# Optimization experiments

Hardware: AMD Instinct MI355X
Metric: run time of the kernel (lower is better)

The kernel has to match this reference:

```python
import jax, jax.numpy as jnp
import numpy as np

H = 128          # hidden_channels
K = 3            # TAGConv hops
NV, NS = 100000, 50000
EVV, ESS, EH, EIN = 1_000_000, 500_000, 500_000, 300_000


def setup_inputs() -> dict:
    key = jax.random.key(0)
    ks = iter(jax.random.split(key, 40))
    def rn(shape, s=0.05):
        return jax.random.normal(next(ks), shape, jnp.float32) * s
    def ri(shape, hi):
        return jax.random.randint(next(ks), shape, 0, hi, jnp.int32)
    return {
        "game_x": rn((NV, 5), 1.0),
        "state_x": rn((NS, 6), 1.0),
        "edge_index_v_v": ri((2, EVV), NV),
        "edge_type_v_v": ri((EVV,), 4),  # unused in forward (interface fidelity)
        "edge_index_history_v_s": jnp.stack([ri((EH,), NV), ri((EH,), NS)]),
        "edge_attr_history_v_s": rn((EH, 1), 1.0),
        "edge_index_in_v_s": jnp.stack([ri((EIN,), NV), ri((EIN,), NS)]),
        "edge_index_s_s": ri((2, ESS), NS),
        # TAGConv weights: (K+1) hop linears, shared bias
        "tag1_W": rn((K + 1, 5, H)), "tag1_b": rn((H,)),
        "tag2_W": rn((K + 1, 6, H)), "tag2_b": rn((H,)),
        # 7 SAGEConv layers stacked: gv[1:3]=0,1; sv[1:3]=2,3; in1=4; sv2=5,6
        "sage_Wl": rn((7, H, H)), "sage_bl": rn((7, H)), "sage_Wr": rn((7, H, H)),
        # GATConv (1 head, edge_dim=1)
        "gat_Wsrc": rn((H, H)), "gat_Wdst": rn((H, H)), "gat_We": rn((1, H)),
        "gat_asrc": rn((H,)), "gat_adst": rn((H,)), "gat_ae": rn((H,)), "gat_b": rn((H,)),
        # final MLP: single Linear(H, 1)
        "mlp_W": rn((H, 1)), "mlp_b": rn((1,)),
    }


def _seg_sum(x, idx, n):
    return jax.ops.segment_sum(x, idx, num_segments=n)


def tag_conv(x, edge_index, n, W, b):
    """TAGConv: out = sum_k lin_k(A_norm^k x) + b, gcn_norm w/o self loops."""
    src, dst = edge_index[0], edge_index[1]
    deg = _seg_sum(jnp.ones(src.shape, x.dtype), dst, n)
    dinv = jnp.where(deg > 0, jax.lax.rsqrt(jnp.maximum(deg, 1.0)), 0.0)
    norm = dinv[src] * dinv[dst]                      # [E]
    out = x @ W[0]
    h = x
    for k in range(1, W.shape[0]):
        h = _seg_sum(h[src] * norm[:, None], dst, n)  # one hop of normalized A
        out = out + h @ W[k]
    return out + b


def sage_conv(x_src, x_dst, edge_index, n_dst, Wl, bl, Wr):
    """SAGEConv(mean): lin_l(mean_j x_src[j]) + lin_r(x_dst)."""
    src, dst = edge_index[0], edge_index[1]
    s = _seg_sum(x_src[src], dst, n_dst)
    cnt = _seg_sum(jnp.ones(src.shape, x_src.dtype), dst, n_dst)
    mean = s / jnp.maximum(cnt, 1.0)[:, None]
    return mean @ Wl + bl + x_dst @ Wr


def gat_conv(x_src, x_dst, edge_index, edge_attr, n_dst,
             Wsrc, Wdst, We, asrc, adst, ae, b):
    """Bipartite GATConv, 1 head, edge features, no self loops."""
    src, dst = edge_index[0], edge_index[1]
    hs = x_src @ Wsrc                                  # [NV, H]
    hd = x_dst @ Wdst                                  # [NS, H]
    a = (hs @ asrc)[src] + (hd @ adst)[dst] + (edge_attr @ We) @ ae  # [E]
    a = jax.nn.leaky_relu(a, 0.2)
    m = jax.ops.segment_max(a, dst, num_segments=n_dst)
    e = jnp.exp(a - m[dst])                            # segment softmax
    denom = _seg_sum(e, dst, n_dst)
    alpha = e / jnp.maximum(denom, 1e-16)[dst]
    out = _seg_sum(alpha[:, None] * hs[src], dst, n_dst)
    return out + b


def reference(game_x, state_x, edge_index_v_v, edge_type_v_v,
              edge_index_history_v_s, edge_attr_history_v_s,
              edge_index_in_v_s, edge_index_s_s,
              tag1_W, tag1_b, tag2_W, tag2_b,
              sage_Wl, sage_bl, sage_Wr,
              gat_Wsrc, gat_Wdst, gat_We, gat_asrc, gat_adst, gat_ae, gat_b,
              mlp_W, mlp_b):
    relu = jax.nn.relu
    nv, ns = game_x.shape[0], state_x.shape[0]
    # game-vertex tower
    gx = relu(tag_conv(game_x, edge_index_v_v, nv, tag1_W, tag1_b))
    for i in range(2):
        gx = relu(sage_conv(gx, gx, edge_index_v_v, nv, sage_Wl[i], sage_bl[i], sage_Wr[i]))
    # state-vertex tower
    sx = relu(tag_conv(state_x, edge_index_s_s, ns, tag2_W, tag2_b))
    for i in range(2, 4):
        sx = relu(sage_conv(sx, sx, edge_index_s_s, ns, sage_Wl[i], sage_bl[i], sage_Wr[i]))
    # bipartite attention game -> state
    hist = relu(gat_conv(gx, sx, edge_index_history_v_s, edge_attr_history_v_s, ns,
                         gat_Wsrc, gat_Wdst, gat_We, gat_asrc, gat_adst, gat_ae, gat_b))
    in_x = relu(sage_conv(gx, hist, edge_index_in_v_s, ns, sage_Wl[4], sage_bl[4], sage_Wr[4]))
    # second state tower
    sx = in_x
    for i in range(5, 7):
        sx = relu(sage_conv(sx, sx, edge_index_s_s, ns, sage_Wl[i], sage_bl[i], sage_Wr[i]))
    return sx @ mlp_W + mlp_b                          # [NS, 1]
```

## Files before the change

### kernel.cpp

```cpp
#include <hip/hip_runtime.h>

#define H 128
typedef unsigned short u16;
typedef __attribute__((ext_vector_type(8))) short bf16x8;
typedef __attribute__((ext_vector_type(4))) float f32x4;


static inline int gridFor(long long work, int block, int cap = 8192){
  long long g = (work + block - 1) / block;
  if (g > cap) g = cap;
  if (g < 1) g = 1;
  return (int)g;
}

__device__ __forceinline__ float waveReduceSum(float v){
  #pragma unroll
  for(int off = 32; off > 0; off >>= 1) v += __shfl_down(v, off);
  return v;
}

__device__ __forceinline__ float bflo(unsigned v){ return __uint_as_float(v << 16); }
__device__ __forceinline__ float bfhi(unsigned v){ return __uint_as_float(v & 0xffff0000u); }
__device__ __forceinline__ u16 f2bf(float f){
  unsigned u = __float_as_uint(f);
  return (u16)((u + 0x7fffu + ((u >> 16) & 1u)) >> 16);
}
__device__ __forceinline__ unsigned pack2(float lo, float hi){
  return (unsigned)f2bf(lo) | ((unsigned)f2bf(hi) << 16);
}

#define BSHIFT 9
#define CH 2048

template<bool HAS_ATTR>
__global__ __launch_bounds__(256) void part_kernel(
    const int* __restrict__ src, const int* __restrict__ dst,
    const float* __restrict__ attr, int* __restrict__ bcur,
    int2* __restrict__ bpairs, float* __restrict__ battr, int E, int cap){
  __shared__ int hist[256];
  __shared__ int hscan[256];
  __shared__ int hbase[256];
  __shared__ int hcur[256];
  __shared__ int2 buf[CH];
  __shared__ float abuf[HAS_ATTR ? CH : 1];

  const int t = threadIdx.x;
  const int e0 = blockIdx.x * CH;
  const int cnt = min(CH, E - e0);

  hist[t] = 0; hcur[t] = 0;
  __syncthreads();

  #pragma unroll
  for(int j = 0; j < 8; j++){
    int i = e0 + j*256 + t;
    if(i - e0 < cnt) atomicAdd(&hist[dst[i] >> BSHIFT], 1);
  }
  __syncthreads();

  {
    int v = hist[t];
    int lane = t & 63, wid = t >> 6;
    int incl = v;
    #pragma unroll
    for(int off = 1; off < 64; off <<= 1){
      int u = __shfl_up(incl, off);
      if(lane >= off) incl += u;
    }
    __shared__ int ws4[4];
    if(lane == 63) ws4[wid] = incl;
    __syncthreads();
    int wofs = 0;
    for(int wj = 0; wj < wid; wj++) wofs += ws4[wj];
    hscan[t] = wofs + incl - v;
    hbase[t] = (v > 0) ? atomicAdd(&bcur[t], v) : 0;
  }
  __syncthreads();

  #pragma unroll
  for(int j = 0; j < 8; j++){
    int i = e0 + j*256 + t;
    if(i - e0 < cnt){
      int d = dst[i], s = src[i];
      int b = d >> BSHIFT;
      int lp = atomicAdd(&hcur[b], 1);
      int slot = hscan[b] + lp;
      buf[slot] = make_int2(d, s);
      if(HAS_ATTR) abuf[slot] = attr[i];
    }
  }
  __syncthreads();

  for(int u = t; u < cnt; u += 256){
    int2 pr = buf[u];
    int b = pr.x >> BSHIFT;
    int g = b * cap + hbase[b] + (u - hscan[b]);
    bpairs[g] = pr;
    if(HAS_ATTR) battr[g] = abuf[u];
  }
}

__global__ void bucket_scan(const int* __restrict__ bcur, int* __restrict__ bbase,
                            int* __restrict__ rp0, int* __restrict__ rp1,
                            int* __restrict__ rp2, int* __restrict__ rp3,
                            int n0, int n1, int n2, int n3){
  int g = blockIdx.x;
  int n = (g == 0) ? n0 : (g == 1) ? n1 : (g == 2) ? n2 : n3;
  int* rowp = (g == 0) ? rp0 : (g == 1) ? rp1 : (g == 2) ? rp2 : rp3;
  int NB = (n + 511) >> BSHIFT;
  int t = threadIdx.x;
  int v = (t < NB) ? bcur[g*256 + t] : 0;
  int lane = t & 63, wid = t >> 6;
  int incl = v;
  #pragma unroll
  for(int off = 1; off < 64; off <<= 1){
    int u = __shfl_up(incl, off);
    if(lane >= off) incl += u;
  }
  __shared__ int ws4[4];
  if(lane == 63) ws4[wid] = incl;
  __syncthreads();
  int wofs = 0;
  for(int wj = 0; wj < wid; wj++) wofs += ws4[wj];
  bbase[g*256 + t] = wofs + incl - v;
  if(t == 0) rowp[n] = ws4[0] + ws4[1] + ws4[2] + ws4[3];
}

template<bool HAS_ATTR, bool DINV>
__global__ __launch_bounds__(256) void build_kernel(
    const int2* __restrict__ bpairs, const float* __restrict__ battr,
    const int* __restrict__ bcur, const int* __restrict__ bbase,
    int* __restrict__ rowp, int* __restrict__ col, float* __restrict__ attrp,
    float* __restrict__ dinv, int cap, int n){
  __shared__ int hist[512];
  __shared__ int hcur[512];
  __shared__ int ws4[4];

  const int b = blockIdx.x;
  const int t = threadIdx.x;
  const int d0 = b << BSHIFT;
  const int dn = min(512, n - d0);
  const int cnt = bcur[b];
  const int base = bbase[b];
  const int2* ep = bpairs + (size_t)b * cap;

  hist[t] = 0; hist[t + 256] = 0;
  __syncthreads();
  for(int u = t; u < cnt; u += 256) atomicAdd(&hist[ep[u].x - d0], 1);
  __syncthreads();

  int a0 = hist[2*t], a1 = hist[2*t + 1];
  int s = a0 + a1;
  int lane = t & 63, wid = t >> 6;
  int incl = s;
  #pragma unroll
  for(int off = 1; off < 64; off <<= 1){
    int u = __shfl_up(incl, off);
    if(lane >= off) incl += u;
  }
  if(lane == 63) ws4[wid] = incl;
  __syncthreads();
  int wofs = 0;
  for(int wj = 0; wj < wid; wj++) wofs += ws4[wj];
  int excl = wofs + incl - s;
  __syncthreads();
  hcur[2*t] = excl; hcur[2*t + 1] = excl + a0;
  if(2*t < dn){
    rowp[d0 + 2*t] = base + excl;
    if(DINV) dinv[d0 + 2*t] = a0 > 0 ? rsqrtf((float)a0) : 0.f;
  }
  if(2*t + 1 < dn){
    rowp[d0 + 2*t + 1] = base + excl + a0;
    if(DINV) dinv[d0 + 2*t + 1] = a1 > 0 ? rsqrtf((float)a1) : 0.f;
  }
  __syncthreads();

  for(int u = t; u < cnt; u += 256){
    int2 pr = ep[u];
    int pos = base + atomicAdd(&hcur[pr.x - d0], 1);
    col[pos] = pr.y;
    if(HAS_ATTR) attrp[pos] = battr[(size_t)b * cap + u];
  }
}


__global__ void cvt_weights(const float* __restrict__ Wl, const float* __restrict__ Wr,
                            const float* __restrict__ Wsrc, u16* __restrict__ Wb){
  const int total = 15 * H * H;
  for(int t = blockIdx.x*blockDim.x + threadIdx.x; t < total; t += gridDim.x*blockDim.x){
    int mat = t >> 14, idx = t & 16383;
    int k = idx >> 7, colj = idx & 127;
    const float* srcp = (mat < 7) ? (Wl + ((size_t)mat << 14))
                       : (mat < 14) ? (Wr + ((size_t)(mat - 7) << 14))
                       : Wsrc;
    Wb[((size_t)mat << 14) + (size_t)colj*H + k] = f2bf(srcp[idx]);
  }
}

__global__ void mat_vec_row(const float* __restrict__ W, const float* __restrict__ a,
                            float* __restrict__ outv){
  int k = threadIdx.x;
  if(k < H){
    float s = 0.f;
    for(int j = 0; j < H; j++) s += W[(size_t)k*H + j] * a[j];
    outv[k] = s;
  }
}

__global__ void dot128(const float* __restrict__ a, const float* __restrict__ b,
                       float* __restrict__ o){
  int l = threadIdx.x;
  float acc = a[l]*b[l] + a[l+64]*b[l+64];
  acc = waveReduceSum(acc);
  if(l == 0) o[0] = acc;
}


template<int C>
__global__ void csr_tag_hop(const int* __restrict__ rowp, const int* __restrict__ col,
                            const float* __restrict__ dinv,
                            const float* __restrict__ hin, int sin,
                            float* __restrict__ hout, int sout, int N){
  for(int i = blockIdx.x*blockDim.x + threadIdx.x; i < N; i += gridDim.x*blockDim.x){
    int b = rowp[i], e = rowp[i+1];
    float dd = dinv[i];
    float acc0[C], acc1[C];
    #pragma unroll
    for(int k = 0; k < C; k++){ acc0[k] = 0.f; acc1[k] = 0.f; }
    int p = b;
    for(; p + 2 <= e; p += 2){
      int s0 = col[p], s1 = col[p+1];
      float n0 = dinv[s0] * dd, n1 = dinv[s1] * dd;
      #pragma unroll
      for(int k = 0; k < C; k++){
        acc0[k] += hin[(size_t)s0*sin + k] * n0;
        acc1[k] += hin[(size_t)s1*sin + k] * n1;
      }
    }
    if(p < e){
      int s0 = col[p];
      float n0 = dinv[s0] * dd;
      #pragma unroll
      for(int k = 0; k < C; k++) acc0[k] += hin[(size_t)s0*sin + k] * n0;
    }
    #pragma unroll
    for(int k = 0; k < C; k++) hout[(size_t)i*sout + k] = acc0[k] + acc1[k];
  }
}

template<int C>
__global__ __launch_bounds__(256) void tag_fuse(
    const float* __restrict__ x, const float* __restrict__ hcat,
    const float* __restrict__ W, const float* __restrict__ bias,
    u16* __restrict__ out, int N){
  __shared__ float Ws[4*C*H];
  for(int u = threadIdx.x; u < 4*C*H; u += 256) Ws[u] = W[u];
  __syncthreads();
  const long long total = (long long)N * H;
  for(long long t = (long long)blockIdx.x*blockDim.x + threadIdx.x; t < total;
      t += (long long)gridDim.x*blockDim.x){
    int i = (int)(t >> 7), j = (int)(t & 127);
    const float* xr = x + (size_t)i*C;
    const float* hr = hcat + (size_t)i*3*C;
    float acc = bias[j];
    #pragma unroll
    for(int k = 0; k < C; k++) acc += xr[k] * Ws[k*H + j];
    #pragma unroll
    for(int k = 0; k < 3*C; k++) acc += hr[k] * Ws[(C + k)*H + j];
    out[t] = f2bf(fmaxf(acc, 0.f));
  }
}


__global__ void csr_gather(const int* __restrict__ rowp, const int* __restrict__ col,
                           const u16* __restrict__ x, u16* __restrict__ agg, int N){
  int lane = threadIdx.x & 63;
  int w = (blockIdx.x*blockDim.x + threadIdx.x) >> 6;
  int nw = (gridDim.x*blockDim.x) >> 6;
  for(int i = w; i < N; i += nw){
    int b = rowp[i], e = rowp[i+1];
    float xs[8], ys[8];
    #pragma unroll
    for(int j = 0; j < 8; j++){ xs[j] = 0.f; ys[j] = 0.f; }
    int p = b;
    for(; p + 8 <= e; p += 8){
      unsigned v[8];
      #pragma unroll
      for(int j = 0; j < 8; j++)
        v[j] = *(const unsigned*)&x[(size_t)col[p + j]*H + lane*2];
      #pragma unroll
      for(int j = 0; j < 8; j++){ xs[j] += bflo(v[j]); ys[j] += bfhi(v[j]); }
    }
    for(; p < e; p++){
      unsigned v = *(const unsigned*)&x[(size_t)col[p]*H + lane*2];
      xs[0] += bflo(v); ys[0] += bfhi(v);
    }
    float sx = (xs[0]+xs[1])+(xs[2]+xs[3])+((xs[4]+xs[5])+(xs[6]+xs[7]));
    float sy = (ys[0]+ys[1])+(ys[2]+ys[3])+((ys[4]+ys[5])+(ys[6]+ys[7]));
    float inv = 1.f / fmaxf((float)(e - b), 1.f);
    *(unsigned*)&agg[(size_t)i*H + lane*2] = pack2(sx*inv, sy*inv);
  }
}


template<bool HAS_AGG, bool RELU, bool BIAS>
__global__ __launch_bounds__(256) void combine_mfma(
    const u16* __restrict__ x, const u16* __restrict__ agg,
    const u16* __restrict__ WbR, const u16* __restrict__ WbL,
    const float* __restrict__ bl, u16* __restrict__ out, int N){
  __shared__ u16 Ws[(HAS_AGG ? 2 : 1) * H * H];

  #pragma unroll
  for(int m = 0; m < (HAS_AGG ? 2 : 1); m++){
    const u16* Wp = m ? WbL : WbR;
    char* dst = (char*)(Ws + m * H * H);
    for(int u = threadIdx.x; u < H * H / 8; u += 256){
      bf16x8 v = *(const bf16x8*)&Wp[u * 8];
      int c  = u >> 4;
      int kb = (u & 15) * 16;
      *(bf16x8*)(dst + c * 256 + (kb ^ ((c & 7) << 4))) = v;
    }
  }
  __syncthreads();

  const int lane = threadIdx.x & 63;
  const int wib  = threadIdx.x >> 6;
  const int m0   = (blockIdx.x * 4 + wib) * 32;
  if(m0 >= N) return;
  const int r16 = lane & 15;
  const int kg  = (lane >> 4) * 8;

  f32x4 acc[2][8];
  #pragma unroll
  for(int rt = 0; rt < 2; rt++)
    #pragma unroll
    for(int t = 0; t < 8; t++) acc[rt][t] = (f32x4){0.f, 0.f, 0.f, 0.f};

  #pragma unroll
  for(int phase = 0; phase < (HAS_AGG ? 2 : 1); phase++){
    const u16* Ap = phase ? agg : x;
    const char* Wbase = (const char*)(Ws + phase * H * H);
    #pragma unroll
    for(int k0 = 0; k0 < H; k0 += 32){
      bf16x8 af[2];
      #pragma unroll
      for(int rt = 0; rt < 2; rt++){
        int row = m0 + rt * 16 + r16;
        if(row < N) af[rt] = *(const bf16x8*)&Ap[(size_t)row * H + k0 + kg];
        else        af[rt] = (bf16x8){0,0,0,0,0,0,0,0};
      }
      #pragma unroll
      for(int t = 0; t < 8; t++){
        int c = t * 16 + r16;
        int kb = (k0 + kg) * 2;
        bf16x8 bf = *(const bf16x8*)(Wbase + c * 256 + (kb ^ ((c & 7) << 4)));
        acc[0][t] = __builtin_amdgcn_mfma_f32_16x16x32_bf16(af[0], bf, acc[0][t], 0, 0, 0);
        acc[1][t] = __builtin_amdgcn_mfma_f32_16x16x32_bf16(af[1], bf, acc[1][t], 0, 0, 0);
      }
    }
  }

  #pragma unroll
  for(int rt = 0; rt < 2; rt++){
    const int orow = m0 + rt * 16 + (lane >> 4) * 4;
    #pragma unroll
    for(int t = 0; t < 8; t++){
      int c = t * 16 + r16;
      float bb = BIAS ? bl[c] : 0.f;
      #pragma unroll
      for(int r = 0; r < 4; r++){
        if(orow + r < N){
          float v = acc[rt][t][r] + bb;
          if(RELU) v = fmaxf(v, 0.f);
          out[(size_t)(orow + r) * H + c] = f2bf(v);
        }
      }
    }
  }
}


__global__ void rowdot_bf(const u16* __restrict__ x, const float* __restrict__ v,
                          float* __restrict__ out, int N){
  int lane = threadIdx.x & 63;
  int w = (blockIdx.x*blockDim.x + threadIdx.x) >> 6;
  int nw = (gridDim.x*blockDim.x) >> 6;
  for(int i = w; i < N; i += nw){
    unsigned u = *(const unsigned*)&x[(size_t)i*H + lane*2];
    float acc = bflo(u)*v[lane*2] + bfhi(u)*v[lane*2 + 1];
    acc = waveReduceSum(acc);
    if(lane == 0) out[i] = acc;
  }
}

__global__ void gat_fused(const int* __restrict__ rowp, const int* __restrict__ colv,
                          const float* __restrict__ attrp, const float* __restrict__ av,
                          const float* __restrict__ ad, const float* __restrict__ cptr,
                          const u16* __restrict__ hs, const float* __restrict__ bias,
                          u16* __restrict__ out, int N){
  const float c = cptr[0];
  int lane = threadIdx.x & 63;
  int w = (blockIdx.x*blockDim.x + threadIdx.x) >> 6;
  int nw = (gridDim.x*blockDim.x) >> 6;
  for(int i = w; i < N; i += nw){
    int b = rowp[i], e = rowp[i+1];
    float adi = ad[i];
    float accx0 = 0.f, accy0 = 0.f, accx1 = 0.f, accy1 = 0.f;
    float sume = 0.f;
    int p = b;
    for(; p + 2 <= e; p += 2){
      int s0 = colv[p], s1 = colv[p+1];
      float a0 = av[s0] + adi + attrp[p] * c;
      float a1 = av[s1] + adi + attrp[p+1] * c;
      a0 = a0 > 0.f ? a0 : 0.2f * a0;
      a1 = a1 > 0.f ? a1 : 0.2f * a1;
      float e0 = __expf(a0), e1 = __expf(a1);
      unsigned v0 = *(const unsigned*)&hs[(size_t)s0*H + lane*2];
      unsigned v1 = *(const unsigned*)&hs[(size_t)s1*H + lane*2];
      accx0 += e0 * bflo(v0); accy0 += e0 * bfhi(v0);
      accx1 += e1 * bflo(v1); accy1 += e1 * bfhi(v1);
      sume += e0 + e1;
    }
    if(p < e){
      int s0 = colv[p];
      float a0 = av[s0] + adi + attrp[p] * c;
      a0 = a0 > 0.f ? a0 : 0.2f * a0;
      float e0 = __expf(a0);
      unsigned v0 = *(const unsigned*)&hs[(size_t)s0*H + lane*2];
      accx0 += e0 * bflo(v0); accy0 += e0 * bfhi(v0);
      sume += e0;
    }
    float rd = 1.f / fmaxf(sume, 1e-16f);
    float ox = fmaxf((accx0 + accx1) * rd + bias[lane*2],     0.f);
    float oy = fmaxf((accy0 + accy1) * rd + bias[lane*2 + 1], 0.f);
    *(unsigned*)&out[(size_t)i*H + lane*2] = pack2(ox, oy);
  }
}

__global__ void mlp_out_bf(const u16* __restrict__ x, const float* __restrict__ W,
                           const float* __restrict__ b, float* __restrict__ out, int N){
  int lane = threadIdx.x & 63;
  int w = (blockIdx.x*blockDim.x + threadIdx.x) >> 6;
  int nw = (gridDim.x*blockDim.x) >> 6;
  for(int i = w; i < N; i += nw){
    unsigned u = *(const unsigned*)&x[(size_t)i*H + lane*2];
    float acc = bflo(u)*W[lane*2] + bfhi(u)*W[lane*2 + 1];
    acc = waveReduceSum(acc);
    if(lane == 0) out[i] = acc + b[0];
  }
}


extern "C" void kernel_launch(void* const* d_in, const int* in_sizes, int n_in,
                              void* d_out, int out_size, void* d_ws, size_t ws_size,
                              hipStream_t stream) {
  const float* game_x  = (const float*)d_in[0];
  const float* state_x = (const float*)d_in[1];
  const int*   e_vv    = (const int*)d_in[2];
  const int*   e_hist  = (const int*)d_in[4];
  const float* attr_h  = (const float*)d_in[5];
  const int*   e_in    = (const int*)d_in[6];
  const int*   e_ss    = (const int*)d_in[7];
  const float* tag1_W  = (const float*)d_in[8];
  const float* tag1_b  = (const float*)d_in[9];
  const float* tag2_W  = (const float*)d_in[10];
  const float* tag2_b  = (const float*)d_in[11];
  const float* sage_Wl = (const float*)d_in[12];
  const float* sage_bl = (const float*)d_in[13];
  const float* sage_Wr = (const float*)d_in[14];
  const float* gat_Wsrc= (const float*)d_in[15];
  const float* gat_Wdst= (const float*)d_in[16];
  const float* gat_We  = (const float*)d_in[17];
  const float* gat_asrc= (const float*)d_in[18];
  const float* gat_adst= (const float*)d_in[19];
  const float* gat_ae  = (const float*)d_in[20];
  const float* gat_b   = (const float*)d_in[21];
  const float* mlp_W   = (const float*)d_in[22];
  const float* mlp_b   = (const float*)d_in[23];
  float* out = (float*)d_out;

  const int NV  = in_sizes[0] / 5;
  const int NS  = in_sizes[1] / 6;
  const int EVV = in_sizes[2] / 2;
  const int EH  = in_sizes[4] / 2;
  const int EIN = in_sizes[6] / 2;
  const int ESS = in_sizes[7] / 2;

  const int* vv_src = e_vv;   const int* vv_dst = e_vv + EVV;
  const int* eh_src = e_hist; const int* eh_dst = e_hist + EH;
  const int* in_src = e_in;   const int* in_dst = e_in + EIN;
  const int* ss_src = e_ss;   const int* ss_dst = e_ss + ESS;

  const int NBv = (NV + 511) >> BSHIFT;
  const int NBs = (NS + 511) >> BSHIFT;
  const int capvv = (EVV / NBv) * 3 / 2 + 64;
  const int capss = (ESS / NBs) * 3 / 2 + 64;
  const int capeh = (EH  / NBs) * 3 / 2 + 64;
  const int capin = (EIN / NBs) * 3 / 2 + 64;

  char* wp = (char*)d_ws;
  auto alloc = [&](size_t bytes) -> void* {
    void* p = (void*)wp;
    wp += (bytes + 511) & ~size_t(511);
    return p;
  };
  u16* V0 = (u16*)alloc((size_t)NV*H*2);
  u16* V1 = (u16*)alloc((size_t)NV*H*2);
  u16* S0 = (u16*)alloc((size_t)NS*H*2);
  u16* S1 = (u16*)alloc((size_t)NS*H*2);
  u16* Wb = (u16*)alloc((size_t)15*H*H*2);
  float* dinv_v = (float*)alloc((size_t)NV*4);
  float* dinv_s = (float*)alloc((size_t)NS*4);
  float* av   = (float*)alloc((size_t)NV*4);
  float* ad   = (float*)alloc((size_t)NS*4);
  float* hcat5= (float*)alloc((size_t)NV*15*4);
  float* hcat6= (float*)alloc((size_t)NS*18*4);
  float* wvec = (float*)alloc(H*4);
  float* cbuf = (float*)alloc(4);
  int* vv_rowp = (int*)alloc((size_t)(NV+1)*4);
  int* vv_col  = (int*)alloc((size_t)EVV*4);
  int* ss_rowp = (int*)alloc((size_t)(NS+1)*4);
  int* ss_col  = (int*)alloc((size_t)ESS*4);
  int* eh_rowp = (int*)alloc((size_t)(NS+1)*4);
  int* eh_col  = (int*)alloc((size_t)EH*4);
  float* eh_attr = (float*)alloc((size_t)EH*4);
  int* in_rowp = (int*)alloc((size_t)(NS+1)*4);
  int* in_col  = (int*)alloc((size_t)EIN*4);
  int2* vv_bp = (int2*)alloc((size_t)NBv*capvv*8);
  int2* ss_bp = (int2*)alloc((size_t)NBs*capss*8);
  int2* eh_bp = (int2*)alloc((size_t)NBs*capeh*8);
  int2* in_bp = (int2*)alloc((size_t)NBs*capin*8);
  float* eh_ba = (float*)alloc((size_t)NBs*capeh*4);
  int* bcur  = (int*)alloc(4*256*4);
  int* bbase = (int*)alloc(4*256*4);
  (void)ws_size; (void)n_in; (void)out_size;

  const int B = 256;
  #define GRID1(n) gridFor((long long)(n), B), B, 0, stream
  #define GRIDW(e) gridFor((long long)(e) * 64, B, 8192), B, 0, stream
  #define GEMM(n)  ((n) + 127) / 128, 256, 0, stream

  hipMemsetAsync(bcur, 0, 4*256*4, stream);
  part_kernel<false><<<(EVV + CH - 1)/CH, 256, 0, stream>>>(
      vv_src, vv_dst, nullptr, bcur + 0,   vv_bp, nullptr, EVV, capvv);
  part_kernel<false><<<(ESS + CH - 1)/CH, 256, 0, stream>>>(
      ss_src, ss_dst, nullptr, bcur + 256, ss_bp, nullptr, ESS, capss);
  part_kernel<true ><<<(EH  + CH - 1)/CH, 256, 0, stream>>>(
      eh_src, eh_dst, attr_h,  bcur + 512, eh_bp, eh_ba,   EH,  capeh);
  part_kernel<false><<<(EIN + CH - 1)/CH, 256, 0, stream>>>(
      in_src, in_dst, nullptr, bcur + 768, in_bp, nullptr, EIN, capin);
  bucket_scan<<<4, 256, 0, stream>>>(bcur, bbase, vv_rowp, ss_rowp, eh_rowp, in_rowp,
                                     NV, NS, NS, NS);
  build_kernel<false,true ><<<NBv, 256, 0, stream>>>(
      vv_bp, nullptr, bcur + 0,   bbase + 0,   vv_rowp, vv_col, nullptr, dinv_v, capvv, NV);
  build_kernel<false,true ><<<NBs, 256, 0, stream>>>(
      ss_bp, nullptr, bcur + 256, bbase + 256, ss_rowp, ss_col, nullptr, dinv_s, capss, NS);
  build_kernel<true ,false><<<NBs, 256, 0, stream>>>(
      eh_bp, eh_ba,   bcur + 512, bbase + 512, eh_rowp, eh_col, eh_attr, nullptr, capeh, NS);
  build_kernel<false,false><<<NBs, 256, 0, stream>>>(
      in_bp, nullptr, bcur + 768, bbase + 768, in_rowp, in_col, nullptr, nullptr, capin, NS);

  cvt_weights<<<GRID1(15*H*H)>>>(sage_Wl, sage_Wr, gat_Wsrc, Wb);
  mat_vec_row<<<1, 128, 0, stream>>>(gat_Wdst, gat_adst, wvec);
  dot128<<<1, 64, 0, stream>>>(gat_We, gat_ae, cbuf);

  #define WBL(l) (Wb + ((size_t)(l) << 14))
  #define WBR(l) (Wb + ((size_t)(7 + (l)) << 14))

  csr_tag_hop<5><<<GRID1(NV)>>>(vv_rowp, vv_col, dinv_v, game_x, 5, hcat5 + 0, 15, NV);
  csr_tag_hop<5><<<GRID1(NV)>>>(vv_rowp, vv_col, dinv_v, hcat5 + 0, 15, hcat5 + 5, 15, NV);
  csr_tag_hop<5><<<GRID1(NV)>>>(vv_rowp, vv_col, dinv_v, hcat5 + 5, 15, hcat5 + 10, 15, NV);
  tag_fuse<5><<<GRID1((long long)NV*H)>>>(game_x, hcat5, tag1_W, tag1_b, V0, NV);

  for(int l = 0; l < 2; l++){
    csr_gather<<<GRIDW(NV)>>>(vv_rowp, vv_col, V0, V1, NV);
    combine_mfma<true,true,true><<<GEMM(NV)>>>(V0, V1, WBR(l), WBL(l),
                                               sage_bl + (size_t)l*H, V0, NV);
  }

  csr_tag_hop<6><<<GRID1(NS)>>>(ss_rowp, ss_col, dinv_s, state_x, 6, hcat6 + 0, 18, NS);
  csr_tag_hop<6><<<GRID1(NS)>>>(ss_rowp, ss_col, dinv_s, hcat6 + 0, 18, hcat6 + 6, 18, NS);
  csr_tag_hop<6><<<GRID1(NS)>>>(ss_rowp, ss_col, dinv_s, hcat6 + 6, 18, hcat6 + 12, 18, NS);
  tag_fuse<6><<<GRID1((long long)NS*H)>>>(state_x, hcat6, tag2_W, tag2_b, S0, NS);

  for(int l = 2; l < 4; l++){
    csr_gather<<<GRIDW(NS)>>>(ss_rowp, ss_col, S0, S1, NS);
    combine_mfma<true,true,true><<<GEMM(NS)>>>(S0, S1, WBR(l), WBL(l),
                                               sage_bl + (size_t)l*H, S0, NS);
  }

  combine_mfma<false,false,false><<<GEMM(NV)>>>(V0, nullptr, Wb + ((size_t)14 << 14),
                                                nullptr, nullptr, V1, NV);
  rowdot_bf<<<GRIDW(NV)>>>(V1, gat_asrc, av, NV);
  rowdot_bf<<<GRIDW(NS)>>>(S0, wvec, ad, NS);
  gat_fused<<<GRIDW(NS)>>>(eh_rowp, eh_col, eh_attr, av, ad, cbuf, V1, gat_b, S1, NS);

  csr_gather<<<GRIDW(NS)>>>(in_rowp, in_col, V0, S0, NS);
  combine_mfma<true,true,true><<<GEMM(NS)>>>(S1, S0, WBR(4), WBL(4),
                                             sage_bl + (size_t)4*H, S1, NS);

  for(int l = 5; l < 7; l++){
    csr_gather<<<GRIDW(NS)>>>(ss_rowp, ss_col, S1, S0, NS);
    combine_mfma<true,true,true><<<GEMM(NS)>>>(S1, S0, WBR(l), WBL(l),
                                               sage_bl + (size_t)l*H, S1, NS);
  }

  mlp_out_bf<<<GRIDW(NS)>>>(S1, mlp_W, mlp_b, out, NS);

  #undef GRID1
  #undef GRIDW
  #undef GEMM
  #undef WBL
  #undef WBR
}
```

Measured before the change: 908.8 us.

## Fuse SAGE neighbor mean-gather into MFMA combine kernel and pad TAG hop buffers

Replaces the separate csr_gather plus combine_mfma pair with a single sage_fused kernel. In it, each MFMA lane gathers and averages its neighbor rows directly into registers, then feeds them to the lin_l MFMA, so the aggregated tensor never goes through global memory. Weights are staged one matrix at a time in a single 32KB LDS buffer to halve shared memory use. The TAG hop outputs move from one interleaved concat buffer to three separate buffers with stride 8, and output ping-pong buffers are rearranged. The risk is that the per-row gather is now serial within 16-lane groups with lower memory parallelism than the wave-per-row gather, and load imbalance across the rows of a wave may stall the MFMA path.

```diff
diff --git a/kernel.cpp b/kernel.cpp
--- a/kernel.cpp
+++ b/kernel.cpp
@@ -220,7 +220,7 @@
 __global__ void csr_tag_hop(const int* __restrict__ rowp, const int* __restrict__ col,
                             const float* __restrict__ dinv,
                             const float* __restrict__ hin, int sin,
-                            float* __restrict__ hout, int sout, int N){
+                            float* __restrict__ hout, int N){
   for(int i = blockIdx.x*blockDim.x + threadIdx.x; i < N; i += gridDim.x*blockDim.x){
     int b = rowp[i], e = rowp[i+1];
     float dd = dinv[i];
@@ -244,13 +244,14 @@
       for(int k = 0; k < C; k++) acc0[k] += hin[(size_t)s0*sin + k] * n0;
     }
     #pragma unroll
-    for(int k = 0; k < C; k++) hout[(size_t)i*sout + k] = acc0[k] + acc1[k];
+    for(int k = 0; k < C; k++) hout[(size_t)i*8 + k] = acc0[k] + acc1[k];
   }
 }
 
 template<int C>
 __global__ __launch_bounds__(256) void tag_fuse(
-    const float* __restrict__ x, const float* __restrict__ hcat,
+    const float* __restrict__ x, const float* __restrict__ h1,
+    const float* __restrict__ h2, const float* __restrict__ h3,
     const float* __restrict__ W, const float* __restrict__ bias,
     u16* __restrict__ out, int N){
   __shared__ float Ws[4*C*H];
@@ -261,119 +262,205 @@
       t += (long long)gridDim.x*blockDim.x){
     int i = (int)(t >> 7), j = (int)(t & 127);
     const float* xr = x + (size_t)i*C;
-    const float* hr = hcat + (size_t)i*3*C;
+    const float* r1 = h1 + (size_t)i*8;
+    const float* r2 = h2 + (size_t)i*8;
+    const float* r3 = h3 + (size_t)i*8;
     float acc = bias[j];
     #pragma unroll
     for(int k = 0; k < C; k++) acc += xr[k] * Ws[k*H + j];
     #pragma unroll
-    for(int k = 0; k < 3*C; k++) acc += hr[k] * Ws[(C + k)*H + j];
+    for(int k = 0; k < C; k++) acc += r1[k] * Ws[(C + k)*H + j];
+    #pragma unroll
+    for(int k = 0; k < C; k++) acc += r2[k] * Ws[(2*C + k)*H + j];
+    #pragma unroll
+    for(int k = 0; k < C; k++) acc += r3[k] * Ws[(3*C + k)*H + j];
     out[t] = f2bf(fmaxf(acc, 0.f));
   }
 }
 
 
-__global__ void csr_gather(const int* __restrict__ rowp, const int* __restrict__ col,
-                           const u16* __restrict__ x, u16* __restrict__ agg, int N){
-  int lane = threadIdx.x & 63;
-  int w = (blockIdx.x*blockDim.x + threadIdx.x) >> 6;
-  int nw = (gridDim.x*blockDim.x) >> 6;
-  for(int i = w; i < N; i += nw){
-    int b = rowp[i], e = rowp[i+1];
-    float xs[8], ys[8];
-    #pragma unroll
-    for(int j = 0; j < 8; j++){ xs[j] = 0.f; ys[j] = 0.f; }
-    int p = b;
-    for(; p + 8 <= e; p += 8){
-      unsigned v[8];
-      #pragma unroll
-      for(int j = 0; j < 8; j++)
-        v[j] = *(const unsigned*)&x[(size_t)col[p + j]*H + lane*2];
-      #pragma unroll
-      for(int j = 0; j < 8; j++){ xs[j] += bflo(v[j]); ys[j] += bfhi(v[j]); }
-    }
-    for(; p < e; p++){
-      unsigned v = *(const unsigned*)&x[(size_t)col[p]*H + lane*2];
-      xs[0] += bflo(v); ys[0] += bfhi(v);
-    }
-    float sx = (xs[0]+xs[1])+(xs[2]+xs[3])+((xs[4]+xs[5])+(xs[6]+xs[7]));
-    float sy = (ys[0]+ys[1])+(ys[2]+ys[3])+((ys[4]+ys[5])+(ys[6]+ys[7]));
-    float inv = 1.f / fmaxf((float)(e - b), 1.f);
-    *(unsigned*)&agg[(size_t)i*H + lane*2] = pack2(sx*inv, sy*inv);
-  }
-}
-
-
-template<bool HAS_AGG, bool RELU, bool BIAS>
-__global__ __launch_bounds__(256) void combine_mfma(
-    const u16* __restrict__ x, const u16* __restrict__ agg,
+__global__ __launch_bounds__(256) void sage_fused(
+    const u16* __restrict__ G, const u16* __restrict__ X,
+    const int* __restrict__ rowp, const int* __restrict__ col,
     const u16* __restrict__ WbR, const u16* __restrict__ WbL,
     const float* __restrict__ bl, u16* __restrict__ out, int N){
-  __shared__ u16 Ws[(HAS_AGG ? 2 : 1) * H * H];
-
-  #pragma unroll
-  for(int m = 0; m < (HAS_AGG ? 2 : 1); m++){
-    const u16* Wp = m ? WbL : WbR;
-    char* dst = (char*)(Ws + m * H * H);
-    for(int u = threadIdx.x; u < H * H / 8; u += 256){
-      bf16x8 v = *(const bf16x8*)&Wp[u * 8];
-      int c  = u >> 4;
-      int kb = (u & 15) * 16;
-      *(bf16x8*)(dst + c * 256 + (kb ^ ((c & 7) << 4))) = v;
-    }
-  }
-  __syncthreads();
-
-  const int lane = threadIdx.x & 63;
-  const int wib  = threadIdx.x >> 6;
-  const int m0   = (blockIdx.x * 4 + wib) * 32;
-  if(m0 >= N) return;
+  __shared__ u16 Ws[H * H];
+
+  const int t = threadIdx.x;
+  const int lane = t & 63;
+  const int wib = t >> 6;
+  const int m0 = (blockIdx.x * 4 + wib) * 32;
   const int r16 = lane & 15;
   const int kg  = (lane >> 4) * 8;
+  const bool active = (m0 < N);
+
+  for(int u = t; u < H*H/8; u += 256){
+    bf16x8 v = *(const bf16x8*)&WbR[u*8];
+    int c = u >> 4, kb = (u & 15) * 16;
+    *(bf16x8*)((char*)Ws + c*256 + (kb ^ ((c & 7) << 4))) = v;
+  }
+  __syncthreads();
 
   f32x4 acc[2][8];
   #pragma unroll
   for(int rt = 0; rt < 2; rt++)
     #pragma unroll
-    for(int t = 0; t < 8; t++) acc[rt][t] = (f32x4){0.f, 0.f, 0.f, 0.f};
-
-  #pragma unroll
-  for(int phase = 0; phase < (HAS_AGG ? 2 : 1); phase++){
-    const u16* Ap = phase ? agg : x;
-    const char* Wbase = (const char*)(Ws + phase * H * H);
-    #pragma unroll
-    for(int k0 = 0; k0 < H; k0 += 32){
+    for(int tt = 0; tt < 8; tt++) acc[rt][tt] = (f32x4){0.f,0.f,0.f,0.f};
+
+  if(active){
+    #pragma unroll
+    for(int k0c = 0; k0c < 4; k0c++){
+      int k0 = k0c * 32;
       bf16x8 af[2];
       #pragma unroll
       for(int rt = 0; rt < 2; rt++){
-        int row = m0 + rt * 16 + r16;
-        if(row < N) af[rt] = *(const bf16x8*)&Ap[(size_t)row * H + k0 + kg];
+        int row = m0 + rt*16 + r16;
+        if(row < N) af[rt] = *(const bf16x8*)&X[(size_t)row*H + k0 + kg];
         else        af[rt] = (bf16x8){0,0,0,0,0,0,0,0};
       }
       #pragma unroll
-      for(int t = 0; t < 8; t++){
-        int c = t * 16 + r16;
-        int kb = (k0 + kg) * 2;
-        bf16x8 bf = *(const bf16x8*)(Wbase + c * 256 + (kb ^ ((c & 7) << 4)));
-        acc[0][t] = __builtin_amdgcn_mfma_f32_16x16x32_bf16(af[0], bf, acc[0][t], 0, 0, 0);
-        acc[1][t] = __builtin_amdgcn_mfma_f32_16x16x32_bf16(af[1], bf, acc[1][t], 0, 0, 0);
+      for(int tt = 0; tt < 8; tt++){
+        int c = tt*16 + r16;
+        int kb = (k0 + kg)*2;
+        bf16x8 bf = *(const bf16x8*)((char*)Ws + c*256 + (kb ^ ((c & 7) << 4)));
+        acc[0][tt] = __builtin_amdgcn_mfma_f32_16x16x32_bf16(af[0], bf, acc[0][tt], 0, 0, 0);
+        acc[1][tt] = __builtin_amdgcn_mfma_f32_16x16x32_bf16(af[1], bf, acc[1][tt], 0, 0, 0);
       }
     }
   }
+  __syncthreads();
+
+  for(int u = t; u < H*H/8; u += 256){
+    bf16x8 v = *(const bf16x8*)&WbL[u*8];
+    int c = u >> 4, kb = (u & 15) * 16;
+    *(bf16x8*)((char*)Ws + c*256 + (kb ^ ((c & 7) << 4))) = v;
+  }
+  __syncthreads();
+
+  if(active){
+    #pragma unroll
+    for(int rt = 0; rt < 2; rt++){
+      int row = m0 + rt*16 + r16;
+      float ag[4][8];
+      #pragma unroll
+      for(int kc = 0; kc < 4; kc++)
+        #pragma unroll
+        for(int j = 0; j < 8; j++) ag[kc][j] = 0.f;
+
+      if(row < N){
+        int b = rowp[row], e = rowp[row+1];
+        for(int p = b; p < e; p++){
+          int s = col[p];
+          const u16* gr = &G[(size_t)s*H + kg];
+          #pragma unroll
+          for(int kc = 0; kc < 4; kc++){
+            bf16x8 v = *(const bf16x8*)(gr + kc*32);
+            const unsigned* vu = (const unsigned*)&v;
+            #pragma unroll
+            for(int q = 0; q < 4; q++){
+              ag[kc][2*q]   += bflo(vu[q]);
+              ag[kc][2*q+1] += bfhi(vu[q]);
+            }
+          }
+        }
+        float inv = 1.f / fmaxf((float)(e - b), 1.f);
+        #pragma unroll
+        for(int kc = 0; kc < 4; kc++)
+          #pragma unroll
+          for(int j = 0; j < 8; j++) ag[kc][j] *= inv;
+      }
+
+      #pragma unroll
+      for(int kc = 0; kc < 4; kc++){
+        unsigned uu[4];
+        #pragma unroll
+        for(int q = 0; q < 4; q++) uu[q] = pack2(ag[kc][2*q], ag[kc][2*q+1]);
+        bf16x8 agb = *(bf16x8*)uu;
+        int kb = (kc*32 + kg)*2;
+        #pragma unroll
+        for(int tt = 0; tt < 8; tt++){
+          int c = tt*16 + r16;
+          bf16x8 bf = *(const bf16x8*)((char*)Ws + c*256 + (kb ^ ((c & 7) << 4)));
+          acc[rt][tt] = __builtin_amdgcn_mfma_f32_16x16x32_bf16(agb, bf, acc[rt][tt], 0, 0, 0);
+        }
+      }
+    }
+
+    #pragma unroll
+    for(int rt = 0; rt < 2; rt++){
+      const int orow = m0 + rt*16 + (lane >> 4) * 4;
+      #pragma unroll
+      for(int tt = 0; tt < 8; tt++){
+        int c = tt*16 + r16;
+        float bb = bl[c];
+        #pragma unroll
+        for(int r = 0; r < 4; r++){
+          if(orow + r < N){
+            float v = fmaxf(acc[rt][tt][r] + bb, 0.f);
+            out[(size_t)(orow + r)*H + c] = f2bf(v);
+          }
+        }
+      }
+    }
+  }
+}
+
+
+__global__ __launch_bounds__(256) void gemm_mfma(
+    const u16* __restrict__ x, const u16* __restrict__ Wb,
+    u16* __restrict__ out, int N){
+  __shared__ u16 Ws[H * H];
+  const int t = threadIdx.x;
+  for(int u = t; u < H*H/8; u += 256){
+    bf16x8 v = *(const bf16x8*)&Wb[u*8];
+    int c = u >> 4, kb = (u & 15) * 16;
+    *(bf16x8*)((char*)Ws + c*256 + (kb ^ ((c & 7) << 4))) = v;
+  }
+  __syncthreads();
+
+  const int lane = t & 63;
+  const int wib = t >> 6;
+  const int m0 = (blockIdx.x * 4 + wib) * 32;
+  if(m0 >= N) return;
+  const int r16 = lane & 15;
+  const int kg = (lane >> 4) * 8;
+
+  f32x4 acc[2][8];
+  #pragma unroll
+  for(int rt = 0; rt < 2; rt++)
+    #pragma unroll
+    for(int tt = 0; tt < 8; tt++) acc[rt][tt] = (f32x4){0.f,0.f,0.f,0.f};
+
+  #pragma unroll
+  for(int k0c = 0; k0c < 4; k0c++){
+    int k0 = k0c * 32;
+    bf16x8 af[2];
+    #pragma unroll
+    for(int rt = 0; rt < 2; rt++){
+      int row = m0 + rt*16 + r16;
+      if(row < N) af[rt] = *(const bf16x8*)&x[(size_t)row*H + k0 + kg];
+      else        af[rt] = (bf16x8){0,0,0,0,0,0,0,0};
+    }
+    #pragma unroll
+    for(int tt = 0; tt < 8; tt++){
+      int c = tt*16 + r16;
+      int kb = (k0 + kg)*2;
+      bf16x8 bf = *(const bf16x8*)((char*)Ws + c*256 + (kb ^ ((c & 7) << 4)));
+      acc[0][tt] = __builtin_amdgcn_mfma_f32_16x16x32_bf16(af[0], bf, acc[0][tt], 0, 0, 0);
+      acc[1][tt] = __builtin_amdgcn_mfma_f32_16x16x32_bf16(af[1], bf, acc[1][tt], 0, 0, 0);
+    }
+  }
 
   #pragma unroll
   for(int rt = 0; rt < 2; rt++){
-    const int orow = m0 + rt * 16 + (lane >> 4) * 4;
-    #pragma unroll
-    for(int t = 0; t < 8; t++){
-      int c = t * 16 + r16;
-      float bb = BIAS ? bl[c] : 0.f;
+    const int orow = m0 + rt*16 + (lane >> 4) * 4;
+    #pragma unroll
+    for(int tt = 0; tt < 8; tt++){
+      int c = tt*16 + r16;
       #pragma unroll
       for(int r = 0; r < 4; r++){
-        if(orow + r < N){
-          float v = acc[rt][t][r] + bb;
-          if(RELU) v = fmaxf(v, 0.f);
-          out[(size_t)(orow + r) * H + c] = f2bf(v);
-        }
+        if(orow + r < N)
+          out[(size_t)(orow + r)*H + c] = f2bf(acc[rt][tt][r]);
       }
     }
   }
@@ -513,8 +600,12 @@
   float* dinv_s = (float*)alloc((size_t)NS*4);
   float* av   = (float*)alloc((size_t)NV*4);
   float* ad   = (float*)alloc((size_t)NS*4);
-  float* hcat5= (float*)alloc((size_t)NV*15*4);
-  float* hcat6= (float*)alloc((size_t)NS*18*4);
+  float* h5a  = (float*)alloc((size_t)NV*8*4);
+  float* h5b  = (float*)alloc((size_t)NV*8*4);
+  float* h5c  = (float*)alloc((size_t)NV*8*4);
+  float* h6a  = (float*)alloc((size_t)NS*8*4);
+  float* h6b  = (float*)alloc((size_t)NS*8*4);
+  float* h6c  = (float*)alloc((size_t)NS*8*4);
   float* wvec = (float*)alloc(H*4);
   float* cbuf = (float*)alloc(4);
   int* vv_rowp = (int*)alloc((size_t)(NV+1)*4);
@@ -567,45 +658,40 @@
   #define WBL(l) (Wb + ((size_t)(l) << 14))
   #define WBR(l) (Wb + ((size_t)(7 + (l)) << 14))
 
-  csr_tag_hop<5><<<GRID1(NV)>>>(vv_rowp, vv_col, dinv_v, game_x, 5, hcat5 + 0, 15, NV);
-  csr_tag_hop<5><<<GRID1(NV)>>>(vv_rowp, vv_col, dinv_v, hcat5 + 0, 15, hcat5 + 5, 15, NV);
-  csr_tag_hop<5><<<GRID1(NV)>>>(vv_rowp, vv_col, dinv_v, hcat5 + 5, 15, hcat5 + 10, 15, NV);
-  tag_fuse<5><<<GRID1((long long)NV*H)>>>(game_x, hcat5, tag1_W, tag1_b, V0, NV);
-
-  for(int l = 0; l < 2; l++){
-    csr_gather<<<GRIDW(NV)>>>(vv_rowp, vv_col, V0, V1, NV);
-    combine_mfma<true,true,true><<<GEMM(NV)>>>(V0, V1, WBR(l), WBL(l),
-                                               sage_bl + (size_t)l*H, V0, NV);
-  }
-
-  csr_tag_hop<6><<<GRID1(NS)>>>(ss_rowp, ss_col, dinv_s, state_x, 6, hcat6 + 0, 18, NS);
-  csr_tag_hop<6><<<GRID1(NS)>>>(ss_rowp, ss_col, dinv_s, hcat6 + 0, 18, hcat6 + 6, 18, NS);
-  csr_tag_hop<6><<<GRID1(NS)>>>(ss_rowp, ss_col, dinv_s, hcat6 + 6, 18, hcat6 + 12, 18, NS);
-  tag_fuse<6><<<GRID1((long long)NS*H)>>>(state_x, hcat6, tag2_W, tag2_b, S0, NS);
-
-  for(int l = 2; l < 4; l++){
-    csr_gather<<<GRIDW(NS)>>>(ss_rowp, ss_col, S0, S1, NS);
-    combine_mfma<true,true,true><<<GEMM(NS)>>>(S0, S1, WBR(l), WBL(l),
-                                               sage_bl + (size_t)l*H, S0, NS);
-  }
-
-  combine_mfma<false,false,false><<<GEMM(NV)>>>(V0, nullptr, Wb + ((size_t)14 << 14),
-                                                nullptr, nullptr, V1, NV);
+  csr_tag_hop<5><<<GRID1(NV)>>>(vv_rowp, vv_col, dinv_v, game_x, 5, h5a, NV);
+  csr_tag_hop<5><<<GRID1(NV)>>>(vv_rowp, vv_col, dinv_v, h5a, 8, h5b, NV);
+  csr_tag_hop<5><<<GRID1(NV)>>>(vv_rowp, vv_col, dinv_v, h5b, 8, h5c, NV);
+  tag_fuse<5><<<GRID1((long long)NV*H)>>>(game_x, h5a, h5b, h5c, tag1_W, tag1_b, V0, NV);
+
+  sage_fused<<<GEMM(NV)>>>(V0, V0, vv_rowp, vv_col, WBR(0), WBL(0),
+                           sage_bl + 0*H, V1, NV);
+  sage_fused<<<GEMM(NV)>>>(V1, V1, vv_rowp, vv_col, WBR(1), WBL(1),
+                           sage_bl + 1*H, V0, NV);
+
+  csr_tag_hop<6><<<GRID1(NS)>>>(ss_rowp, ss_col, dinv_s, state_x, 6, h6a, NS);
+  csr_tag_hop<6><<<GRID1(NS)>>>(ss_rowp, ss_col, dinv_s, h6a, 8, h6b, NS);
+  csr_tag_hop<6><<<GRID1(NS)>>>(ss_rowp, ss_col, dinv_s, h6b, 8, h6c, NS);
+  tag_fuse<6><<<GRID1((long long)NS*H)>>>(state_x, h6a, h6b, h6c, tag2_W, tag2_b, S0, NS);
+
+  sage_fused<<<GEMM(NS)>>>(S0, S0, ss_rowp, ss_col, WBR(2), WBL(2),
+                           sage_bl + 2*H, S1, NS);
+  sage_fused<<<GEMM(NS)>>>(S1, S1, ss_rowp, ss_col, WBR(3), WBL(3),
+                           sage_bl + 3*H, S0, NS);
+
+  gemm_mfma<<<GEMM(NV)>>>(V0, Wb + ((size_t)14 << 14), V1, NV);
   rowdot_bf<<<GRIDW(NV)>>>(V1, gat_asrc, av, NV);
   rowdot_bf<<<GRIDW(NS)>>>(S0, wvec, ad, NS);
   gat_fused<<<GRIDW(NS)>>>(eh_rowp, eh_col, eh_attr, av, ad, cbuf, V1, gat_b, S1, NS);
 
-  csr_gather<<<GRIDW(NS)>>>(in_rowp, in_col, V0, S0, NS);
-  combine_mfma<true,true,true><<<GEMM(NS)>>>(S1, S0, WBR(4), WBL(4),
-                                             sage_bl + (size_t)4*H, S1, NS);
-
-  for(int l = 5; l < 7; l++){
-    csr_gather<<<GRIDW(NS)>>>(ss_rowp, ss_col, S1, S0, NS);
-    combine_mfma<true,true,true><<<GEMM(NS)>>>(S1, S0, WBR(l), WBL(l),
-                                               sage_bl + (size_t)l*H, S1, NS);
-  }
-
-  mlp_out_bf<<<GRIDW(NS)>>>(S1, mlp_W, mlp_b, out, NS);
+  sage_fused<<<GEMM(NS)>>>(V0, S1, in_rowp, in_col, WBR(4), WBL(4),
+                           sage_bl + 4*H, S0, NS);
+
+  sage_fused<<<GEMM(NS)>>>(S0, S0, ss_rowp, ss_col, WBR(5), WBL(5),
+                           sage_bl + 5*H, S1, NS);
+  sage_fused<<<GEMM(NS)>>>(S1, S1, ss_rowp, ss_col, WBR(6), WBL(6),
+                           sage_bl + 6*H, S0, NS);
+
+  mlp_out_bf<<<GRIDW(NS)>>>(S0, mlp_W, mlp_b, out, NS);
 
   #undef GRID1
   #undef GRIDW
```

New measurement: 898.2 us. About the same (-1.2%).
